# Optimization experiments

Hardware: AMD Instinct MI355X
Metric: run time of the kernel (lower is better)

## Reference

```python
import jax, jax.numpy as jnp
import numpy as np

THETA = 10000.0  # RoPE base


def _rope(x):
    # x: [B, T, H] with H even. Matches torch view_as_complex on (..., H//2, 2)
    # pairing of adjacent elements, rotated by m * theta_i.
    B, T, H = x.shape
    inv_freq = 1.0 / (THETA ** (jnp.arange(0, H, 2, dtype=jnp.float32) / H))  # [H/2]
    ang = jnp.arange(T, dtype=jnp.float32)[:, None] * inv_freq[None, :]       # [T, H/2]
    cos, sin = jnp.cos(ang), jnp.sin(ang)
    xr = x.astype(jnp.float32).reshape(B, T, H // 2, 2)
    a, b = xr[..., 0], xr[..., 1]
    out = jnp.stack([a * cos - b * sin, a * sin + b * cos], axis=-1)          # complex mult
    return out.reshape(B, T, H).astype(x.dtype)


def setup_inputs() -> dict:
    key = jax.random.key(0)
    k1, k2, k3, k4 = jax.random.split(key, 4)
    B, T, C, H = 4, 4096, 1024, 64
    return {
        "x": jax.random.normal(k1, (B, T, C), dtype=jnp.float32),
        "wq": jax.random.normal(k2, (C, H), dtype=jnp.float32) * 0.02,
        "wk": jax.random.normal(k3, (C, H), dtype=jnp.float32) * 0.02,
        "wv": jax.random.normal(k4, (C, H), dtype=jnp.float32) * 0.02,
    }


def reference(x, wq, wk, wv):
    # Head.forward, training branch; dropout is identity (eval determinism).
    B, T, C = x.shape
    H = wq.shape[1]
    q = _rope(x @ wq)   # [B, T, H]
    k = _rope(x @ wk)   # [B, T, H]
    v = x @ wv          # [B, T, H]
    wei = jnp.einsum('bqh,bkh->bqk', q, k) * (H ** -0.5)   # [B, T, T]
    causal = jnp.tril(jnp.ones((T, T), dtype=bool))
    wei = jnp.where(causal, wei, -jnp.inf)
    wei = jax.nn.softmax(wei, axis=-1)
    out = jnp.einsum('bqk,bkh->bqh', wei, v)               # [B, T, H]
    return out
```

## Files before the change

### kernel.cpp

```cpp
#include <hip/hip_runtime.h>
#include <hip/hip_bf16.h>
#include <math.h>

#define B_ 4
#define T_ 4096
#define C_ 1024
#define H_ 64
#define ROWS_ (B_*T_)

typedef __attribute__((ext_vector_type(8))) short bf16x8;
typedef __attribute__((ext_vector_type(4))) float f32x4;

__device__ __forceinline__ unsigned short f2bf(float f) {
    union { float f; unsigned u; } x; x.f = f;
    unsigned r = x.u + 0x7fffu + ((x.u >> 16) & 1u);
    return (unsigned short)(r >> 16);
}
__device__ __forceinline__ float bf2f(unsigned short s) {
    union { unsigned u; float f; } x; x.u = ((unsigned)s) << 16;
    return x.f;
}
__device__ __forceinline__ unsigned pk2bf(float a, float b) {
    __hip_bfloat162 h = __float22bfloat162_rn(float2{a, b});
    return *reinterpret_cast<unsigned*>(&h);
}
__device__ __forceinline__ void gld16(const void* g, void* l) {
    __builtin_amdgcn_global_load_lds(
        (const __attribute__((address_space(1))) unsigned*)g,
        (__attribute__((address_space(3))) unsigned*)l, 16, 0, 0);
}

__global__ __launch_bounds__(256) void prep_kernel(
    const float* __restrict__ wq, const float* __restrict__ wk,
    const float* __restrict__ wv, unsigned short* __restrict__ wt,
    float* __restrict__ tab)
{
    __shared__ float ts[64][68];
    const int tid = threadIdx.x;
    if (blockIdx.x < 48) {
        const int m  = blockIdx.x >> 4;
        const int k0 = (blockIdx.x & 15) * 64;
        const float* w = (m == 0) ? wq : (m == 1) ? wk : wv;
        {
            const int r = tid >> 2;
            const int c = (tid & 3) * 16;
            #pragma unroll
            for (int i = 0; i < 4; ++i)
                *reinterpret_cast<float4*>(&ts[r][c + 4*i]) =
                    *reinterpret_cast<const float4*>(&w[(size_t)(k0 + r)*H_ + c + 4*i]);
        }
        __syncthreads();
        {
            const int n  = tid >> 2;
            const int kc = (tid & 3) * 16;
            unsigned short outp[16];
            #pragma unroll
            for (int j = 0; j < 16; ++j) outp[j] = f2bf(ts[kc + j][n]);
            unsigned short* dst = &wt[((size_t)m*64 + n)*C_ + k0 + kc];
            *reinterpret_cast<uint4*>(dst)     = *reinterpret_cast<uint4*>(&outp[0]);
            *reinterpret_cast<uint4*>(dst + 8) = *reinterpret_cast<uint4*>(&outp[8]);
        }
    } else {
        const int idx = (blockIdx.x - 48)*256 + tid;
        const int t   = idx >> 5;
        const int hp  = idx & 31;
        const float inv = __builtin_exp2f(-(float)hp * (13.287712379549449f / 32.f));
        float sn, cs;
        sincosf((float)t * inv, &sn, &cs);
        *reinterpret_cast<float2*>(&tab[2*idx]) = float2{cs, sn};
    }
}

__global__ __launch_bounds__(256, 2) void qkv_mfma_kernel(
    const float* __restrict__ x, const unsigned short* __restrict__ wt,
    const float* __restrict__ tab,
    unsigned short* __restrict__ qb, unsigned short* __restrict__ kb,
    unsigned short* __restrict__ vtb)
{
    __shared__ unsigned short SM[28672];

    const int tid  = threadIdx.x;
    const int w    = tid >> 6;
    const int lane = tid & 63;
    const int rt   = w >> 1;
    const int ch   = w & 1;
    const int lr   = lane & 15;
    const int lg   = lane >> 4;
    const int rb   = blockIdx.x * 32;

    const int ar = tid >> 3;
    const int ac = (tid & 7) * 8;

    float4 axr[2];

    auto load_A = [&](int t) {
        const float* p = &x[(size_t)(rb + ar)*C_ + t*64 + ac];
        axr[0] = *reinterpret_cast<const float4*>(p);
        axr[1] = *reinterpret_cast<const float4*>(p + 4);
    };
    auto write_A = [&](int buf) {
        unsigned tmp[4];
        tmp[0] = pk2bf(axr[0].x, axr[0].y);
        tmp[1] = pk2bf(axr[0].z, axr[0].w);
        tmp[2] = pk2bf(axr[1].x, axr[1].y);
        tmp[3] = pk2bf(axr[1].z, axr[1].w);
        const int off = buf*4096 + ar*128 + ((ac*2) ^ ((ar & 7) << 4));
        *reinterpret_cast<uint4*>((char*)SM + off) = *reinterpret_cast<uint4*>(tmp);
    };
    auto stage_W = [&](int t, int buf) {
        #pragma unroll
        for (int s = 0; s < 6; ++s) {
            const int slot = s*256 + tid;
            const int r    = slot >> 3;
            const int c8   = (slot & 7) * 8;
            const int c8s  = c8 ^ ((r & 7) << 3);
            gld16(&wt[(size_t)r*C_ + t*64 + c8s],
                  (char*)SM + 8192 + buf*24576 + slot*16);
        }
    };

    f32x4 acc[6];
    #pragma unroll
    for (int j = 0; j < 6; ++j) acc[j] = f32x4{0.f, 0.f, 0.f, 0.f};

    load_A(0);
    stage_W(0, 0);
    write_A(0);
    load_A(1);

    for (int t = 0; t < 16; ++t) {
        const int cur = t & 1, nxt = cur ^ 1;
        __syncthreads();
        if (t < 15) { stage_W(t + 1, nxt); write_A(nxt); }
        if (t < 14) load_A(t + 2);
        char* Acur = (char*)SM + cur*4096;
        char* Wcur = (char*)SM + 8192 + cur*24576;
        #pragma unroll
        for (int kh = 0; kh < 2; ++kh) {
            const int arow = rt*16 + lr;
            bf16x8 af = *reinterpret_cast<const bf16x8*>(
                Acur + arow*128 + ((kh*64 + lg*16) ^ ((arow & 7) << 4)));
            #pragma unroll
            for (int j = 0; j < 6; ++j) {
                const int n = ch*96 + j*16 + lr;
                bf16x8 bf = *reinterpret_cast<const bf16x8*>(
                    Wcur + n*128 + ((kh*64 + lg*16) ^ ((n & 7) << 4)));
                acc[j] = __builtin_amdgcn_mfma_f32_16x16x32_bf16(af, bf, acc[j], 0, 0, 0);
            }
        }
    }

    __syncthreads();
    const int rl0  = rt*16 + lg*4;
    const int row0 = rb + rl0;
    #pragma unroll
    for (int j = 0; j < 6; ++j) {
        const int c = ch*96 + j*16 + lr;
        const int m = c >> 6;
        const int h = c & 63;
        if (m < 2) {
            const int base_ls = (m == 0) ? 0 : 2048;
            const float qs = (m == 0) ? 0.125f : 1.0f;
            const int hp = h >> 1;
            #pragma unroll
            for (int i = 0; i < 4; ++i) {
                const float v  = acc[j][i];
                const float pr = __shfl_xor(v, 1);
                if (!(h & 1)) {
                    const int tp = (row0 + i) & (T_ - 1);
                    const float2 cssn = *reinterpret_cast<const float2*>(
                        &tab[((size_t)tp*32 + hp)*2]);
                    const float oe = (v*cssn.x - pr*cssn.y) * qs;
                    const float oo = (v*cssn.y + pr*cssn.x) * qs;
                    *reinterpret_cast<unsigned*>(&SM[base_ls + (rl0 + i)*64 + h]) =
                        pk2bf(oe, oo);
                }
            }
        } else {
            unsigned short pk[4];
            #pragma unroll
            for (int i = 0; i < 4; ++i) pk[i] = f2bf(acc[j][i]);
            char* vbase = (char*)SM + 8192 + h*64;
            *reinterpret_cast<uint2*>(vbase + ((rl0*2) ^ ((h & 7) << 3))) =
                *reinterpret_cast<uint2*>(pk);
        }
    }
    __syncthreads();
    {
        const int row = tid >> 3;
        const int h0  = (tid & 7) * 8;
        *reinterpret_cast<uint4*>(&qb[(size_t)(rb + row)*H_ + h0]) =
            *reinterpret_cast<const uint4*>(&SM[row*64 + h0]);
        *reinterpret_cast<uint4*>(&kb[(size_t)(rb + row)*H_ + h0]) =
            *reinterpret_cast<const uint4*>(&SM[2048 + row*64 + h0]);
        const int h  = tid >> 2;
        const int t0 = (tid & 3) * 8;
        char* vbase = (char*)SM + 8192 + h*64;
        uint2 a  = *reinterpret_cast<uint2*>(vbase + (((t0*2)    ) ^ ((h & 7) << 3)));
        uint2 b2 = *reinterpret_cast<uint2*>(vbase + (((t0*2) + 8) ^ ((h & 7) << 3)));
        const int bh  = (rb >> 12)*64 + h;
        const int tp0 = rb & (T_ - 1);
        uint4 o; o.x = a.x; o.y = a.y; o.z = b2.x; o.w = b2.y;
        *reinterpret_cast<uint4*>(&vtb[(size_t)bh*T_ + tp0 + t0]) = o;
    }
}

__global__ __launch_bounds__(256, 3) void attn_chunk_kernel(
    const unsigned short* __restrict__ qb, const unsigned short* __restrict__ kb,
    const unsigned short* __restrict__ vtb,
    unsigned short* __restrict__ partO, float* __restrict__ partML,
    int CH, int per_batch)
{
    __shared__ unsigned short Kls[2][4096];
    __shared__ unsigned short Vls[2][4096];
    __shared__ unsigned short Pls[4][2048];

    const int tid  = threadIdx.x;
    const int w    = tid >> 6;
    const int lane = tid & 63;
    const int lr   = lane & 15;
    const int lg   = lane >> 4;

    const int cid = blockIdx.x;
    const int b   = cid / per_batch;
    int r0 = cid - b*per_batch;
    const int G = CH >> 1;
    int a = 0, off = 0;
    while (r0 >= off + G*(a + 1)) { off += G*(a + 1); ++a; }
    const int idx = r0 - off;
    const int qt  = G*a + idx/(a + 1);
    const int c   = idx % (a + 1);

    const int q0  = qt * 128;
    const int kt0 = c * CH;
    const int ntk = 2*qt + 2;
    const int ns  = min(kt0 + CH, ntk) - kt0;
    const size_t rbase = (size_t)b * T_;
    const int dtile = 2*qt + (w >> 1);

    char* Pw = (char*)&Pls[w][0];

    bf16x8 qf[2][2];
    #pragma unroll
    for (int s16 = 0; s16 < 2; ++s16) {
        const unsigned short* qp = qb + (rbase + q0 + w*32 + s16*16 + lr)*H_ + lg*8;
        qf[s16][0] = *reinterpret_cast<const bf16x8*>(qp);
        qf[s16][1] = *reinterpret_cast<const bf16x8*>(qp + 32);
    }

    float mrow[2] = {-1e30f, -1e30f};
    float lrow[2] = {0.f, 0.f};
    f32x4 acc[2][4];
    #pragma unroll
    for (int s16 = 0; s16 < 2; ++s16)
        #pragma unroll
        for (int hs = 0; hs < 4; ++hs) acc[s16][hs] = f32x4{0.f, 0.f, 0.f, 0.f};

    const int srow = tid >> 3;
    const int scol = (tid & 7) * 8;
    auto stage_dma = [&](int kt, int buf) {
        #pragma unroll
        for (int s = 0; s < 2; ++s) {
            const int r    = s*32 + srow;
            const int c8s  = scol ^ ((r & 7) << 3);
            const int slot = s*256 + tid;
            gld16(&kb[(rbase + (size_t)kt*64 + r)*H_ + c8s],
                  (char*)&Kls[buf][0] + slot*16);
            gld16(&vtb[((size_t)(b*64 + r))*T_ + (size_t)kt*64 + c8s],
                  (char*)&Vls[buf][0] + slot*16);
        }
    };

    stage_dma(kt0, 0);

    for (int s = 0; s < ns; ++s) {
        __syncthreads();
        if (s + 1 < ns) stage_dma(kt0 + s + 1, (s + 1) & 1);
        const int kt = kt0 + s;
        char* Kb = (char*)&Kls[s & 1][0];
        char* Vb = (char*)&Vls[s & 1][0];

        if (kt <= dtile) {
            f32x4 st[2][4];
            __builtin_amdgcn_s_setprio(1);
            #pragma unroll
            for (int ks = 0; ks < 4; ++ks) {
                const int rr2 = ks*16 + lr;
                const int sw  = (rr2 & 7) << 4;
                bf16x8 kf0 = *reinterpret_cast<const bf16x8*>(Kb + rr2*128 + ((lg*16     ) ^ sw));
                bf16x8 kf1 = *reinterpret_cast<const bf16x8*>(Kb + rr2*128 + ((lg*16 + 64) ^ sw));
                #pragma unroll
                for (int s16 = 0; s16 < 2; ++s16) {
                    f32x4 t = {0.f, 0.f, 0.f, 0.f};
                    t = __builtin_amdgcn_mfma_f32_16x16x32_bf16(kf0, qf[s16][0], t, 0, 0, 0);
                    t = __builtin_amdgcn_mfma_f32_16x16x32_bf16(kf1, qf[s16][1], t, 0, 0, 0);
                    st[s16][ks] = t;
                }
            }
            __builtin_amdgcn_s_setprio(0);

            float scl[2];
            const int swp = (lr & 7) << 4;
            #pragma unroll
            for (int s16 = 0; s16 < 2; ++s16) {
                const int qg = q0 + w*32 + s16*16 + lr;
                float mx = -1e30f;
                if (kt == dtile) {
                    #pragma unroll
                    for (int ks = 0; ks < 4; ++ks)
                        #pragma unroll
                        for (int i = 0; i < 4; ++i) {
                            const int kg = kt*64 + ks*16 + lg*4 + i;
                            const float v = (kg <= qg) ? st[s16][ks][i] : -1e30f;
                            st[s16][ks][i] = v;
                            mx = fmaxf(mx, v);
                        }
                } else {
                    #pragma unroll
                    for (int ks = 0; ks < 4; ++ks)
                        #pragma unroll
                        for (int i = 0; i < 4; ++i) mx = fmaxf(mx, st[s16][ks][i]);
                }
                mx = fmaxf(mx, __shfl_xor(mx, 16));
                mx = fmaxf(mx, __shfl_xor(mx, 32));
                const float mn = fmaxf(mrow[s16], mx);
                scl[s16] = __expf(mrow[s16] - mn);
                float ls = 0.f;
                #pragma unroll
                for (int ks = 0; ks < 4; ++ks)
                    #pragma unroll
                    for (int i = 0; i < 4; ++i) {
                        const float p = __expf(st[s16][ks][i] - mn);
                        st[s16][ks][i] = p;
                        ls += p;
                    }
                ls += __shfl_xor(ls, 16);
                ls += __shfl_xor(ls, 32);
                lrow[s16] = lrow[s16]*scl[s16] + ls;
                mrow[s16] = mn;

                const int pr = s16*16 + lr;
                #pragma unroll
                for (int ks = 0; ks < 4; ++ks) {
                    const unsigned u0 = pk2bf(st[s16][ks][0], st[s16][ks][1]);
                    const unsigned u1 = pk2bf(st[s16][ks][2], st[s16][ks][3]);
                    *reinterpret_cast<uint2*>(Pw + pr*128 + ((ks*32 + lg*8) ^ swp)) =
                        make_uint2(u0, u1);
                }
            }

            #pragma unroll
            for (int s16 = 0; s16 < 2; ++s16) {
                float sclr[4];
                #pragma unroll
                for (int i = 0; i < 4; ++i) sclr[i] = __shfl(scl[s16], lg*4 + i);
                #pragma unroll
                for (int hs = 0; hs < 4; ++hs)
                    #pragma unroll
                    for (int i = 0; i < 4; ++i) acc[s16][hs][i] *= sclr[i];
            }

            bf16x8 pf[2][2];
            #pragma unroll
            for (int s16 = 0; s16 < 2; ++s16) {
                const int pr = s16*16 + lr;
                pf[s16][0] = *reinterpret_cast<const bf16x8*>(Pw + pr*128 + ((lg*16     ) ^ swp));
                pf[s16][1] = *reinterpret_cast<const bf16x8*>(Pw + pr*128 + ((lg*16 + 64) ^ swp));
            }
            __builtin_amdgcn_s_setprio(1);
            #pragma unroll
            for (int hs = 0; hs < 4; ++hs) {
                const int rv  = hs*16 + lr;
                const int swv = (rv & 7) << 4;
                bf16x8 vf0 = *reinterpret_cast<const bf16x8*>(Vb + rv*128 + ((lg*16     ) ^ swv));
                bf16x8 vf1 = *reinterpret_cast<const bf16x8*>(Vb + rv*128 + ((lg*16 + 64) ^ swv));
                #pragma unroll
                for (int s16 = 0; s16 < 2; ++s16) {
                    acc[s16][hs] = __builtin_amdgcn_mfma_f32_16x16x32_bf16(pf[s16][0], vf0, acc[s16][hs], 0, 0, 0);
                    acc[s16][hs] = __builtin_amdgcn_mfma_f32_16x16x32_bf16(pf[s16][1], vf1, acc[s16][hs], 0, 0, 0);
                }
            }
            __builtin_amdgcn_s_setprio(0);
        }
    }

    #pragma unroll
    for (int s16 = 0; s16 < 2; ++s16) {
        const int myrow = w*32 + s16*16 + lr;
        if (lg == 0) {
            partML[(size_t)cid*256 + myrow]       = mrow[s16];
            partML[(size_t)cid*256 + 128 + myrow] = lrow[s16];
        }
    }
    __syncthreads();
    unsigned short* Ols = &Kls[0][0];
    #pragma unroll
    for (int s16 = 0; s16 < 2; ++s16)
        #pragma unroll
        for (int hs = 0; hs < 4; ++hs)
            #pragma unroll
            for (int i = 0; i < 4; ++i)
                Ols[(w*32 + s16*16 + lg*4 + i)*64 + hs*16 + lr] =
                    f2bf(acc[s16][hs][i]);
    __syncthreads();
    {
        const int e0 = tid * 32;
        #pragma unroll
        for (int j = 0; j < 4; ++j)
            *reinterpret_cast<uint4*>(&partO[(size_t)cid*8192 + e0 + 8*j]) =
                *reinterpret_cast<const uint4*>(&Ols[e0 + 8*j]);
    }
}

__global__ __launch_bounds__(256) void combine_kernel(
    const unsigned short* __restrict__ partO, const float* __restrict__ partML,
    float* __restrict__ out, int CH, int per_batch)
{
    const int bq   = blockIdx.x;
    const int b    = bq >> 6;
    const int qt   = (bq >> 1) & 31;
    const int half = bq & 1;
    const int G  = CH >> 1;
    const int a  = qt / G;
    const int nc = a + 1;
    const int cb = b*per_batch + (G*a*(a + 1))/2 + (qt - G*a)*(a + 1);

    const int tid = threadIdx.x;
    const int row = half*64 + (tid >> 2);
    const int h0  = (tid & 3) * 16;

    float mi[8], wi[8];
    float M = -1e30f;
    #pragma unroll
    for (int i = 0; i < 8; ++i) if (i < nc) {
        mi[i] = partML[(size_t)(cb + i)*256 + row];
        M = fmaxf(M, mi[i]);
    }
    float L = 0.f;
    #pragma unroll
    for (int i = 0; i < 8; ++i) if (i < nc) {
        wi[i] = __expf(mi[i] - M);
        L += partML[(size_t)(cb + i)*256 + 128 + row] * wi[i];
    }
    const float inv = 1.f / L;

    float o[16];
    #pragma unroll
    for (int j = 0; j < 16; ++j) o[j] = 0.f;
    #pragma unroll
    for (int i = 0; i < 8; ++i) if (i < nc) {
        const unsigned short* p = &partO[(size_t)(cb + i)*8192 + (size_t)row*64 + h0];
        uint4 u0 = *reinterpret_cast<const uint4*>(p);
        uint4 u1 = *reinterpret_cast<const uint4*>(p + 8);
        const unsigned* uu = (const unsigned*)&u0;
        #pragma unroll
        for (int j = 0; j < 4; ++j) {
            o[2*j]   += bf2f((unsigned short)(uu[j] & 0xffffu)) * wi[i];
            o[2*j+1] += bf2f((unsigned short)(uu[j] >> 16))     * wi[i];
        }
        const unsigned* uv = (const unsigned*)&u1;
        #pragma unroll
        for (int j = 0; j < 4; ++j) {
            o[8+2*j]   += bf2f((unsigned short)(uv[j] & 0xffffu)) * wi[i];
            o[8+2*j+1] += bf2f((unsigned short)(uv[j] >> 16))     * wi[i];
        }
    }
    float* op = &out[((size_t)b*T_ + (size_t)qt*128 + row)*H_ + h0];
    #pragma unroll
    for (int j = 0; j < 4; ++j) {
        float4 v = make_float4(o[4*j]*inv, o[4*j+1]*inv, o[4*j+2]*inv, o[4*j+3]*inv);
        *reinterpret_cast<float4*>(op + 4*j) = v;
    }
}

extern "C" void kernel_launch(void* const* d_in, const int* in_sizes, int n_in,
                              void* d_out, int out_size, void* d_ws, size_t ws_size,
                              hipStream_t stream) {
    const float* x  = (const float*)d_in[0];
    const float* wq = (const float*)d_in[1];
    const float* wk = (const float*)d_in[2];
    const float* wv = (const float*)d_in[3];
    float* out = (float*)d_out;

    unsigned short* qb  = (unsigned short*)d_ws;
    unsigned short* kb  = qb  + (size_t)ROWS_ * H_;
    unsigned short* vtb = kb  + (size_t)ROWS_ * H_;
    unsigned short* wt  = vtb + (size_t)ROWS_ * H_;

    const size_t fixed = (size_t)3*ROWS_*H_*2 + (size_t)3*64*C_*2;
    const size_t need8 = fixed + (size_t)576*8192*2 + (size_t)576*256*4;
    int CH, per_batch;
    if (ws_size >= need8) { CH = 8;  per_batch = 144; }
    else                  { CH = 16; per_batch = 80; }
    const int nblk = 4 * per_batch;

    unsigned short* partO  = wt + (size_t)3*64*C_;
    float*          partML = (float*)(partO + (size_t)nblk*8192);

    float* rope_tab = (float*)partO;

    prep_kernel<<<560, 256, 0, stream>>>(wq, wk, wv, wt, rope_tab);
    qkv_mfma_kernel<<<ROWS_/32, 256, 0, stream>>>(x, wt, rope_tab, qb, kb, vtb);
    attn_chunk_kernel<<<nblk, 256, 0, stream>>>(qb, kb, vtb, partO, partML,
                                                CH, per_batch);
    combine_kernel<<<256, 256, 0, stream>>>(partO, partML, out, CH, per_batch);
}
```

Baseline: 73.38 us.

## Triple-buffer K/V staging with prefetch depth two and vmcnt-based waits

The attention chunk kernel now keeps three K/V LDS buffers in one unified shared array and prefetches two tiles ahead. The blanket __syncthreads is replaced by a partial s_waitcnt vmcnt(4) plus a raw s_barrier, so the oldest tile can be consumed while the next tile's loads are still in flight. This aims to hide more global-load latency behind the MFMA work. The larger LDS footprint (64 KB) forces launch bounds down from 3 to 2 blocks per CU, which reduces occupancy.

```diff
diff --git a/kernel.cpp b/kernel.cpp
--- a/kernel.cpp
+++ b/kernel.cpp
@@ -205,15 +205,13 @@
     }
 }
 
-__global__ __launch_bounds__(256, 3) void attn_chunk_kernel(
+__global__ __launch_bounds__(256, 2) void attn_chunk_kernel(
     const unsigned short* __restrict__ qb, const unsigned short* __restrict__ kb,
     const unsigned short* __restrict__ vtb,
     unsigned short* __restrict__ partO, float* __restrict__ partML,
     int CH, int per_batch)
 {
-    __shared__ unsigned short Kls[2][4096];
-    __shared__ unsigned short Vls[2][4096];
-    __shared__ unsigned short Pls[4][2048];
+    __shared__ unsigned short SM[32768];
 
     const int tid  = threadIdx.x;
     const int w    = tid >> 6;
@@ -238,7 +236,7 @@
     const size_t rbase = (size_t)b * T_;
     const int dtile = 2*qt + (w >> 1);
 
-    char* Pw = (char*)&Pls[w][0];
+    char* Pw = (char*)SM + 49152 + w*4096;
 
     bf16x8 qf[2][2];
     #pragma unroll
@@ -260,25 +258,30 @@
     const int scol = (tid & 7) * 8;
     auto stage_dma = [&](int kt, int buf) {
         #pragma unroll
-        for (int s = 0; s < 2; ++s) {
-            const int r    = s*32 + srow;
+        for (int s2 = 0; s2 < 2; ++s2) {
+            const int r    = s2*32 + srow;
             const int c8s  = scol ^ ((r & 7) << 3);
-            const int slot = s*256 + tid;
+            const int slot = s2*256 + tid;
             gld16(&kb[(rbase + (size_t)kt*64 + r)*H_ + c8s],
-                  (char*)&Kls[buf][0] + slot*16);
+                  (char*)SM + buf*8192 + slot*16);
             gld16(&vtb[((size_t)(b*64 + r))*T_ + (size_t)kt*64 + c8s],
-                  (char*)&Vls[buf][0] + slot*16);
+                  (char*)SM + 24576 + buf*8192 + slot*16);
         }
     };
 
     stage_dma(kt0, 0);
+    if (1 < ns) stage_dma(kt0 + 1, 1);
 
     for (int s = 0; s < ns; ++s) {
-        __syncthreads();
-        if (s + 1 < ns) stage_dma(kt0 + s + 1, (s + 1) & 1);
+        if (s + 1 < ns) asm volatile("s_waitcnt vmcnt(4)" ::: "memory");
+        else            asm volatile("s_waitcnt vmcnt(0)" ::: "memory");
+        __builtin_amdgcn_s_barrier();
+        __builtin_amdgcn_sched_barrier(0);
+        if (s + 2 < ns) stage_dma(kt0 + s + 2, (s + 2) % 3);
+
         const int kt = kt0 + s;
-        char* Kb = (char*)&Kls[s & 1][0];
-        char* Vb = (char*)&Vls[s & 1][0];
+        char* Kb = (char*)SM + (s % 3)*8192;
+        char* Vb = (char*)SM + 24576 + (s % 3)*8192;
 
         if (kt <= dtile) {
             f32x4 st[2][4];
@@ -393,7 +396,7 @@
         }
     }
     __syncthreads();
-    unsigned short* Ols = &Kls[0][0];
+    unsigned short* Ols = &SM[0];
     #pragma unroll
     for (int s16 = 0; s16 < 2; ++s16)
         #pragma unroll
```

New measurement: 77.57 us. 5.7% more time.
